# Kernel optimization log

Hardware: AMD Instinct MI355X
Metric: run time of the kernel (lower is better)

## Reference

```python
import jax, jax.numpy as jnp
import numpy as np

IH, IW = 32, 32
HEADS = 8
DIM_HEAD = 64
SCALE = DIM_HEAD ** -0.5


def _make_relative_index():
    # Matches torch buffer: ceil Euclidean distance between all pairs of 2D coords.
    ii, jj = np.meshgrid(np.arange(IH), np.arange(IW), indexing='ij')
    coords = np.stack([ii.ravel(), jj.ravel()])  # [2, n]
    rel = coords[:, :, None] - coords[:, None, :]  # [2, n, n]
    dist = np.ceil(np.sqrt(rel[0] ** 2 + rel[1] ** 2))
    return jnp.asarray(dist.astype(np.int32).ravel())  # [n*n]


def setup_inputs() -> dict:
    key = jax.random.key(0)
    k1, k2, k3, k4 = jax.random.split(key, 4)
    b, n, inp = 32, IH * IW, 512
    inner = HEADS * DIM_HEAD
    diag = int(np.ceil(np.sqrt((IH - 1) ** 2 + (IW - 1) ** 2)))
    return {
        'x': jax.random.normal(k1, (b, n, inp), jnp.float32),
        'w_qkv': jax.random.normal(k2, (inp, inner * 3), jnp.float32) * (inp ** -0.5),
        'bias_table': jax.random.normal(k3, (diag + 1, HEADS), jnp.float32) * 0.02,
        'w_out': jax.random.normal(k4, (inner, 512), jnp.float32) * (inner ** -0.5),
        'b_out': jnp.zeros((512,), jnp.float32),
        'relative_index': _make_relative_index(),
    }


def reference(x, w_qkv, bias_table, w_out, b_out, relative_index):
    b, n, _ = x.shape
    qkv = x @ w_qkv  # [b, n, 3*inner]
    q, k, v = jnp.split(qkv, 3, axis=-1)
    def to_heads(t):
        return t.reshape(b, n, HEADS, DIM_HEAD).transpose(0, 2, 1, 3)  # b h n d
    q, k, v = to_heads(q), to_heads(k), to_heads(v)
    dots = jnp.einsum('bhid,bhjd->bhij', q, k) * SCALE  # [b, h, n, n]
    # gather relative bias: [n*n, h] -> [1, h, n, n]
    rel_bias = bias_table[relative_index].reshape(n, n, HEADS).transpose(2, 0, 1)
    attn = jax.nn.softmax(dots + rel_bias[None], axis=-1)
    out = jnp.einsum('bhij,bhjd->bhid', attn, v)  # b h n d
    out = out.transpose(0, 2, 1, 3).reshape(b, n, HEADS * DIM_HEAD)
    return out @ w_out + b_out
```

## Files before the change

kernel.cpp:

```cpp
#include <hip/hip_runtime.h>
#include <hip/hip_bf16.h>
#include <cstdint>

typedef __bf16 bf16_t;
typedef bf16_t bf16x8 __attribute__((ext_vector_type(8)));
typedef float f32x4 __attribute__((ext_vector_type(4)));
typedef float f32x16 __attribute__((ext_vector_type(16)));
typedef unsigned u32x4 __attribute__((ext_vector_type(4)));

#define MFMA16(a, b, c) __builtin_amdgcn_mfma_f32_16x16x32_bf16(a, b, c, 0, 0, 0)
#define MFMA32(a, b, c) __builtin_amdgcn_mfma_f32_32x32x16_bf16(a, b, c, 0, 0, 0)

constexpr int LDK = 72;

#define QSCALE 0.1803368801f
#define LOG2E 1.44269504f

__global__ void zero_out(unsigned short* __restrict__ out, long n) {
    long i = (long)blockIdx.x * 256 + threadIdx.x;
    if (i < n) out[i] = 0;
}

__global__ void detect_dtype(const unsigned* __restrict__ x,
                             int* __restrict__ flag) {
    if (threadIdx.x == 0 && blockIdx.x == 0) {
        int cnt = 0;
        for (int i = 0; i < 1024; ++i) {
            unsigned e = (x[i] >> 7) & 0xFF;
            cnt += (e > 100 && e < 150) ? 1 : 0;
        }
        *flag = (cnt > 512) ? 1 : 0;
    }
}

__global__ void transpose_flex(const void* __restrict__ in,
                               bf16_t* __restrict__ out, int R, int C,
                               const int* __restrict__ flagp, int scale_rows) {
    const int fl = *flagp;
    __shared__ bf16_t tile[32][33];
    int c0 = blockIdx.x * 32, r0 = blockIdx.y * 32;
    int x = threadIdx.x, y = threadIdx.y;
#pragma unroll
    for (int i = 0; i < 4; ++i) {
        long idx = (long)(r0 + y + 8 * i) * C + c0 + x;
        float fv = fl ? (float)((const bf16_t*)in)[idx]
                      : ((const float*)in)[idx];
        if (c0 + x < scale_rows) fv *= QSCALE;
        tile[y + 8 * i][x] = (bf16_t)fv;
    }
    __syncthreads();
#pragma unroll
    for (int i = 0; i < 4; ++i)
        out[(long)(c0 + y + 8 * i) * R + r0 + x] = tile[x][y + 8 * i];
}

__global__ __launch_bounds__(256) void build_bias_perm(
    const int* __restrict__ rel_index, const void* __restrict__ bias_table,
    bf16_t* __restrict__ perm, const int* __restrict__ flagp) {
    const int fl = *flagp;
    const int jt = blockIdx.x;
    const int qb = blockIdx.y;
    const int t = threadIdx.x;
    const int lane = t & 63;
    const int h = (t >> 6) + 4 * blockIdx.z;
    const int i = qb * 32 + (lane & 31);
    const int hi = lane >> 5;
    bf16_t out[16];
#pragma unroll
    for (int r = 0; r < 16; ++r) {
        int j = jt * 32 + (r & 3) + 8 * (r >> 2) + 4 * hi;
        int ridx = rel_index[i * 1024 + j];
        ridx = ridx < 0 ? 0 : (ridx > 44 ? 44 : ridx);
        float bv = fl ? (float)((const bf16_t*)bias_table)[ridx * 8 + h]
                      : ((const float*)bias_table)[ridx * 8 + h];
        out[r] = (bf16_t)(bv * LOG2E);
    }
    long off = (((long)(h * 32 + qb) * 32 + jt) << 10) + lane * 16;
    *(uint4*)&perm[off] = *(uint4*)&out[0];
    *(uint4*)&perm[off + 8] = *(uint4*)&out[8];
}

template <bool AFLEX, bool BIAS, bool OUTFLEX>
__global__ __launch_bounds__(256) void gemm128(
    const void* __restrict__ A, const bf16_t* __restrict__ Bt, int K, int lda,
    long a_row0, void* __restrict__ C, int ldc, long c_row0,
    const void* __restrict__ bias, const int* __restrict__ flagp) {
    const int fl = *flagp;
    __shared__ bf16_t a_lds[128 * LDK];
    __shared__ bf16_t b_lds[128 * LDK];
    int t = threadIdx.x;
    int wave = t >> 6, lane = t & 63;
    int m16 = lane & 15, quad = lane >> 4;
    int wr = wave >> 1, wc = wave & 1;
    long m0 = (long)blockIdx.y * 128;
    int n0 = blockIdx.x * 128;

    f32x4 acc[4][4] = {};

    for (int ks = 0; ks < K; ks += 64) {
#pragma unroll
        for (int i = 0; i < 4; ++i) {
            int c = t + 256 * i;
            int row = c >> 3;
            int kc = (c & 7) << 3;
            bf16x8 av;
            if (AFLEX && !fl) {
                const float* Af = (const float*)A;
                long base = (a_row0 + m0 + row) * (long)lda + ks + kc;
                f32x4 lo = *(const f32x4*)&Af[base];
                f32x4 hi = *(const f32x4*)&Af[base + 4];
#pragma unroll
                for (int e = 0; e < 4; ++e) {
                    av[e] = (bf16_t)lo[e];
                    av[e + 4] = (bf16_t)hi[e];
                }
            } else {
                av = *(const bf16x8*)&(
                    (const bf16_t*)A)[(a_row0 + m0 + row) * (long)lda + ks + kc];
            }
            *(bf16x8*)&a_lds[row * LDK + kc] = av;
            *(bf16x8*)&b_lds[row * LDK + kc] =
                *(const bf16x8*)&Bt[(long)(n0 + row) * K + ks + kc];
        }
        __syncthreads();
#pragma unroll
        for (int kf = 0; kf < 2; ++kf) {
            bf16x8 af[4], bfr[4];
#pragma unroll
            for (int mb = 0; mb < 4; ++mb)
                af[mb] = *(const bf16x8*)&a_lds[(wr * 64 + mb * 16 + m16) * LDK +
                                                kf * 32 + quad * 8];
#pragma unroll
            for (int nb = 0; nb < 4; ++nb)
                bfr[nb] = *(const bf16x8*)&b_lds[(wc * 64 + nb * 16 + m16) * LDK +
                                                 kf * 32 + quad * 8];
#pragma unroll
            for (int mb = 0; mb < 4; ++mb)
#pragma unroll
                for (int nb = 0; nb < 4; ++nb)
                    acc[mb][nb] = MFMA16(af[mb], bfr[nb], acc[mb][nb]);
        }
        __syncthreads();
    }

#pragma unroll
    for (int mb = 0; mb < 4; ++mb) {
#pragma unroll
        for (int nb = 0; nb < 4; ++nb) {
            int col = n0 + wc * 64 + nb * 16 + m16;
#pragma unroll
            for (int r = 0; r < 4; ++r) {
                long row = m0 + wr * 64 + mb * 16 + quad * 4 + r;
                float v = acc[mb][nb][r];
                if (BIAS) {
                    float bb = fl ? (float)((const bf16_t*)bias)[col]
                                  : ((const float*)bias)[col];
                    v += bb;
                }
                long off = (c_row0 + row) * (long)ldc + col;
                if (OUTFLEX && !fl)
                    ((float*)C)[off] = v;
                else
                    ((bf16_t*)C)[off] = (bf16_t)v;
            }
        }
    }
}

__global__ __launch_bounds__(256) void flash_attn2(
    bf16_t* __restrict__ qkv, const bf16_t* __restrict__ bias_perm) {
    __shared__ bf16_t k_lds[2][64 * 64];
    __shared__ bf16_t v_lds[2][64 * 64];

    const int t = threadIdx.x;
    const int lane = t & 63, wave = t >> 6;
    const int l31 = lane & 31, hi = lane >> 5;
    const int h = blockIdx.y, b = blockIdx.z;
    bf16_t* base = qkv + (long)b * 1024 * 1536;
    bf16_t* qb = base + h * 64;
    const bf16_t* kb = base + 512 + h * 64;
    const bf16_t* vb = base + 1024 + h * 64;
    const int qblk = blockIdx.x * 4 + wave;
    const int q0w = qblk * 32;
    const bf16_t* bp = bias_perm + (((long)(h * 32 + qblk)) << 15) + lane * 16;

    bf16x8 qf[4];
#pragma unroll
    for (int s = 0; s < 4; ++s)
        qf[s] = *(const bf16x8*)&qb[(long)(q0w + l31) * 1536 + s * 16 + hi * 8];

    f32x16 oacc0 = {}, oacc1 = {};
    float mrun = -1e30f, lrun = 0.f;

    const int sr0 = t >> 3, sg0 = t & 7;
    const int sr1 = sr0 + 32;

    {
        bf16x8 k0 = *(const bf16x8*)&kb[(long)sr0 * 1536 + sg0 * 8];
        bf16x8 k1 = *(const bf16x8*)&kb[(long)sr1 * 1536 + sg0 * 8];
        bf16x8 v0 = *(const bf16x8*)&vb[(long)sr0 * 1536 + sg0 * 8];
        bf16x8 v1 = *(const bf16x8*)&vb[(long)sr1 * 1536 + sg0 * 8];
        *(bf16x8*)&k_lds[0][sr0 * 64 + ((sg0 ^ (sr0 & 7)) << 3)] = k0;
        *(bf16x8*)&k_lds[0][sr1 * 64 + ((sg0 ^ (sr1 & 7)) << 3)] = k1;
#pragma unroll
        for (int e = 0; e < 8; ++e) {
            int d0 = sg0 * 8 + e;
            v_lds[0][d0 * 64 + (((sr0 >> 3) ^ (d0 & 7)) << 3) + (sr0 & 7)] = v0[e];
            v_lds[0][d0 * 64 + (((sr1 >> 3) ^ (d0 & 7)) << 3) + (sr1 & 7)] = v1[e];
        }
    }
    __syncthreads();

    for (int tt = 0; tt < 16; ++tt) {
        const int cur = tt & 1;
        bf16x8 kn0 = {}, kn1 = {}, vn0 = {}, vn1 = {};
        if (tt < 15) {
            long j0n = (long)(tt + 1) * 64;
            kn0 = *(const bf16x8*)&kb[(j0n + sr0) * 1536 + sg0 * 8];
            kn1 = *(const bf16x8*)&kb[(j0n + sr1) * 1536 + sg0 * 8];
            vn0 = *(const bf16x8*)&vb[(j0n + sr0) * 1536 + sg0 * 8];
            vn1 = *(const bf16x8*)&vb[(j0n + sr1) * 1536 + sg0 * 8];
        }
        const bf16_t* bt = bp + ((long)tt << 11);
        uint4 bv[4];
        bv[0] = *(const uint4*)(bt);
        bv[1] = *(const uint4*)(bt + 8);
        bv[2] = *(const uint4*)(bt + 1024);
        bv[3] = *(const uint4*)(bt + 1024 + 8);

#pragma unroll
        for (int js = 0; js < 2; ++js) {
            f32x16 s = {};
            const int krow = js * 32 + l31;
#pragma unroll
            for (int st = 0; st < 4; ++st) {
                bf16x8 kf = *(const bf16x8*)&k_lds[cur][krow * 64 +
                             (((st * 2 + hi) ^ (krow & 7)) << 3)];
                s = MFMA32(kf, qf[st], s);
            }
            bf16_t bb[16];
            *(uint4*)&bb[0] = bv[2 * js];
            *(uint4*)&bb[8] = bv[2 * js + 1];
            float sv[16];
#pragma unroll
            for (int r = 0; r < 16; ++r) sv[r] = s[r] + (float)bb[r];
            float mx = sv[0];
#pragma unroll
            for (int r = 1; r < 16; ++r) mx = fmaxf(mx, sv[r]);
            {
                float o0 = mx, o1 = mx;
                asm("" : "+v"(o1));
                asm("v_permlane32_swap_b32 %0, %1" : "+v"(o0), "+v"(o1));
                mx = fmaxf(o0, o1);
            }
            if (!__all(mx <= mrun + 11.0f)) {
                float mnew = fmaxf(mrun, mx);
                float al = __builtin_amdgcn_exp2f(mrun - mnew);
                mrun = mnew;
                lrun *= al;
#pragma unroll
                for (int r = 0; r < 16; ++r) {
                    oacc0[r] *= al;
                    oacc1[r] *= al;
                }
            }
            float s0 = 0.f, s1 = 0.f, s2 = 0.f, s3 = 0.f;
#pragma unroll
            for (int r = 0; r < 16; ++r) {
                sv[r] = __builtin_amdgcn_exp2f(sv[r] - mrun);
                if ((r & 3) == 0) s0 += sv[r];
                else if ((r & 3) == 1) s1 += sv[r];
                else if ((r & 3) == 2) s2 += sv[r];
                else s3 += sv[r];
            }
            float rs = (s0 + s1) + (s2 + s3);
            {
                float o0 = rs, o1 = rs;
                asm("" : "+v"(o1));
                asm("v_permlane32_swap_b32 %0, %1" : "+v"(o0), "+v"(o1));
                rs = o0 + o1;
            }
            lrun += rs;
            unsigned dw[8];
#pragma unroll
            for (int g = 0; g < 4; ++g) {
                unsigned da, db;
                asm("v_cvt_pk_bf16_f32 %0, %1, %2"
                    : "=v"(da) : "v"(sv[4 * g]), "v"(sv[4 * g + 1]));
                asm("v_cvt_pk_bf16_f32 %0, %1, %2"
                    : "=v"(db) : "v"(sv[4 * g + 2]), "v"(sv[4 * g + 3]));
                dw[2 * g] = da;
                dw[2 * g + 1] = db;
            }
#pragma unroll
            for (int kk = 0; kk < 2; ++kk) {
                asm("v_permlane32_swap_b32 %0, %1"
                    : "+v"(dw[4 * kk + 0]), "+v"(dw[4 * kk + 2]));
                asm("v_permlane32_swap_b32 %0, %1"
                    : "+v"(dw[4 * kk + 1]), "+v"(dw[4 * kk + 3]));
            }
#pragma unroll
            for (int kk = 0; kk < 2; ++kk) {
                u32x4 uv;
                uv[0] = dw[4 * kk + 0];
                uv[1] = dw[4 * kk + 1];
                uv[2] = dw[4 * kk + 2];
                uv[3] = dw[4 * kk + 3];
                bf16x8 pa = __builtin_bit_cast(bf16x8, uv);
#pragma unroll
                for (int db2 = 0; db2 < 2; ++db2) {
                    const int vrow = db2 * 32 + l31;
                    bf16x8 vf = *(const bf16x8*)&v_lds[cur][vrow * 64 +
                                 (((js * 4 + kk * 2 + hi) ^ (vrow & 7)) << 3)];
                    if (db2 == 0)
                        oacc0 = MFMA32(pa, vf, oacc0);
                    else
                        oacc1 = MFMA32(pa, vf, oacc1);
                }
            }
        }
        if (tt < 15) {
            const int nb = cur ^ 1;
            *(bf16x8*)&k_lds[nb][sr0 * 64 + ((sg0 ^ (sr0 & 7)) << 3)] = kn0;
            *(bf16x8*)&k_lds[nb][sr1 * 64 + ((sg0 ^ (sr1 & 7)) << 3)] = kn1;
#pragma unroll
            for (int e = 0; e < 8; ++e) {
                int d0 = sg0 * 8 + e;
                v_lds[nb][d0 * 64 + (((sr0 >> 3) ^ (d0 & 7)) << 3) + (sr0 & 7)] =
                    vn0[e];
                v_lds[nb][d0 * 64 + (((sr1 >> 3) ^ (d0 & 7)) << 3) + (sr1 & 7)] =
                    vn1[e];
            }
        }
        __syncthreads();
    }

    float linv = 1.0f / lrun;
#pragma unroll
    for (int r = 0; r < 16; ++r) {
        int row = (r & 3) + 8 * (r >> 2) + 4 * hi;
        float lr = __int_as_float(
            __builtin_amdgcn_ds_bpermute(row << 2, __float_as_int(linv)));
        qb[(long)(q0w + row) * 1536 + l31] = (bf16_t)(oacc0[r] * lr);
        qb[(long)(q0w + row) * 1536 + 32 + l31] = (bf16_t)(oacc1[r] * lr);
    }
}

extern "C" void kernel_launch(void* const* d_in, const int* in_sizes, int n_in,
                              void* d_out, int out_size, void* d_ws,
                              size_t ws_size, hipStream_t stream) {
    const void* x = nullptr;
    const void* w_qkv = nullptr;
    const void* bias_table = nullptr;
    const void* w_out = nullptr;
    const void* b_out = nullptr;
    const void* rel_raw = nullptr;
    for (int i = 0; i < n_in; ++i) {
        switch (in_sizes[i]) {
            case 16777216: x = d_in[i]; break;
            case 786432:  w_qkv = d_in[i]; break;
            case 360:     bias_table = d_in[i]; break;
            case 262144:  w_out = d_in[i]; break;
            case 512:     b_out = d_in[i]; break;
            case 1048576: rel_raw = d_in[i]; break;
            default: break;
        }
    }
    if (!x || !w_qkv || !bias_table || !w_out || !b_out || !rel_raw) {
        x = d_in[0]; w_qkv = d_in[1]; bias_table = d_in[2];
        w_out = d_in[3]; b_out = d_in[4]; rel_raw = d_in[5];
    }
    const int* rel_index = (const int*)rel_raw;

    char* ws = (char*)d_ws;
    bf16_t* wqkvT = (bf16_t*)ws;
    bf16_t* woutT = (bf16_t*)(ws + 1572864);
    int* flag = (int*)(ws + 1572864 + 524288);
    bf16_t* rel_bias = (bf16_t*)(ws + 1572864 + 524288 + 256);
    const size_t fixed = 1572864 + 524288 + 256 + 16777216;
    bf16_t* qkv = (bf16_t*)(ws + fixed);
    const size_t per_batch = (size_t)1024 * 1536 * sizeof(bf16_t);

    if (ws_size < fixed + per_batch) {
        long n = (long)out_size;
        long nblk = (n + 255) / 256;
        if (nblk > 0)
            zero_out<<<(unsigned)nblk, 256, 0, stream>>>(
                (unsigned short*)d_out, n);
        return;
    }

    size_t avail = ws_size - fixed;
    int chunk = (int)(avail / per_batch);
    if (chunk > 32) chunk = 32;
    if (chunk < 1) chunk = 1;
    while (32 % chunk) --chunk;

    detect_dtype<<<1, 64, 0, stream>>>((const unsigned*)x, flag);
    transpose_flex<<<dim3(1536 / 32, 512 / 32), dim3(32, 8), 0, stream>>>(
        w_qkv, wqkvT, 512, 1536, flag, 512);
    transpose_flex<<<dim3(512 / 32, 512 / 32), dim3(32, 8), 0, stream>>>(
        w_out, woutT, 512, 512, flag, 0);
    build_bias_perm<<<dim3(32, 32, 2), 256, 0, stream>>>(
        rel_index, bias_table, rel_bias, flag);

    for (int b0 = 0; b0 < 32; b0 += chunk) {
        long row0 = (long)b0 * 1024;
        int mrows = chunk * 1024;
        gemm128<true, false, false>
            <<<dim3(1536 / 128, mrows / 128), 256, 0, stream>>>(
                x, wqkvT, 512, 512, row0, qkv, 1536, 0, nullptr, flag);
        flash_attn2<<<dim3(8, 8, chunk), 256, 0, stream>>>(qkv, rel_bias);
        gemm128<false, true, true>
            <<<dim3(512 / 128, mrows / 128), 256, 0, stream>>>(
                qkv, woutT, 512, 1536, 0, d_out, 512, row0, b_out, flag);
    }
}
```

Before: 503.2 us.

## Pre-convert x to bf16 and use direct global-to-LDS loads in GEMMs

Measured after the change: 474.2 us. 5.8% less time.

```diff
diff --git a/kernel.cpp b/kernel.cpp
--- a/kernel.cpp
+++ b/kernel.cpp
@@ -10,6 +10,11 @@
 
 #define MFMA16(a, b, c) __builtin_amdgcn_mfma_f32_16x16x32_bf16(a, b, c, 0, 0, 0)
 #define MFMA32(a, b, c) __builtin_amdgcn_mfma_f32_32x32x16_bf16(a, b, c, 0, 0, 0)
+
+#define GLOAD_LDS16(g, l)                                                  \
+    __builtin_amdgcn_global_load_lds(                                      \
+        (const __attribute__((address_space(1))) unsigned*)(g),            \
+        (__attribute__((address_space(3))) unsigned*)(l), 16, 0, 0)
 
 constexpr int LDK = 72;
 
@@ -30,6 +35,26 @@
             cnt += (e > 100 && e < 150) ? 1 : 0;
         }
         *flag = (cnt > 512) ? 1 : 0;
+    }
+}
+
+__global__ __launch_bounds__(256) void convert_x(const void* __restrict__ in,
+                                                 bf16_t* __restrict__ out,
+                                                 const int* __restrict__ flagp) {
+    const int fl = *flagp;
+    long i = ((long)blockIdx.x * 256 + threadIdx.x) * 8;
+    if (fl) {
+        *(bf16x8*)&out[i] = *(const bf16x8*)&((const bf16_t*)in)[i];
+    } else {
+        f32x4 lo = *(const f32x4*)&((const float*)in)[i];
+        f32x4 hi = *(const f32x4*)&((const float*)in)[i + 4];
+        bf16x8 v;
+#pragma unroll
+        for (int e = 0; e < 4; ++e) {
+            v[e] = (bf16_t)lo[e];
+            v[e + 4] = (bf16_t)hi[e];
+        }
+        *(bf16x8*)&out[i] = v;
     }
 }
 
@@ -78,6 +103,81 @@
     long off = (((long)(h * 32 + qb) * 32 + jt) << 10) + lane * 16;
     *(uint4*)&perm[off] = *(uint4*)&out[0];
     *(uint4*)&perm[off + 8] = *(uint4*)&out[8];
+}
+
+template <bool BIAS, bool OUTFLEX>
+__global__ __launch_bounds__(256) void gemm_lds(
+    const bf16_t* __restrict__ A, const bf16_t* __restrict__ Bt, int K,
+    int lda, long a_row0, void* __restrict__ C, int ldc, long c_row0,
+    const void* __restrict__ bias, const int* __restrict__ flagp) {
+    const int fl = *flagp;
+    __shared__ bf16_t a_lds[128 * 64];
+    __shared__ bf16_t b_lds[128 * 64];
+    int t = threadIdx.x;
+    int wave = t >> 6, lane = t & 63;
+    int m16 = lane & 15, quad = lane >> 4;
+    int wr = wave >> 1, wc = wave & 1;
+    long m0 = (long)blockIdx.y * 128;
+    int n0 = blockIdx.x * 128;
+
+    const int c_base = wave * 256 + lane;
+
+    f32x4 acc[4][4] = {};
+
+    for (int ks = 0; ks < K; ks += 64) {
+#pragma unroll
+        for (int i = 0; i < 4; ++i) {
+            int c = c_base;
+            c = wave * 256 + i * 64 + lane;
+            int row = c >> 3, kc = (c & 7) << 3;
+            GLOAD_LDS16(&A[(a_row0 + m0 + row) * (long)lda + ks + kc],
+                        &a_lds[row * 64 + kc]);
+            GLOAD_LDS16(&Bt[(long)(n0 + row) * K + ks + kc],
+                        &b_lds[row * 64 + kc]);
+        }
+        __syncthreads();
+#pragma unroll
+        for (int kf = 0; kf < 2; ++kf) {
+            bf16x8 af[4], bfr[4];
+#pragma unroll
+            for (int mb = 0; mb < 4; ++mb)
+                af[mb] = *(const bf16x8*)&a_lds[(wr * 64 + mb * 16 + m16) * 64 +
+                                                kf * 32 + quad * 8];
+#pragma unroll
+            for (int nb = 0; nb < 4; ++nb)
+                bfr[nb] = *(const bf16x8*)&b_lds[(wc * 64 + nb * 16 + m16) * 64 +
+                                                 kf * 32 + quad * 8];
+#pragma unroll
+            for (int mb = 0; mb < 4; ++mb)
+#pragma unroll
+                for (int nb = 0; nb < 4; ++nb)
+                    acc[mb][nb] = MFMA16(af[mb], bfr[nb], acc[mb][nb]);
+        }
+        __syncthreads();
+    }
+
+#pragma unroll
+    for (int mb = 0; mb < 4; ++mb) {
+#pragma unroll
+        for (int nb = 0; nb < 4; ++nb) {
+            int col = n0 + wc * 64 + nb * 16 + m16;
+#pragma unroll
+            for (int r = 0; r < 4; ++r) {
+                long row = m0 + wr * 64 + mb * 16 + quad * 4 + r;
+                float v = acc[mb][nb][r];
+                if (BIAS) {
+                    float bb = fl ? (float)((const bf16_t*)bias)[col]
+                                  : ((const float*)bias)[col];
+                    v += bb;
+                }
+                long off = (c_row0 + row) * (long)ldc + col;
+                if (OUTFLEX && !fl)
+                    ((float*)C)[off] = v;
+                else
+                    ((bf16_t*)C)[off] = (bf16_t)v;
+            }
+        }
+    }
 }
 
 template <bool AFLEX, bool BIAS, bool OUTFLEX>
@@ -378,7 +478,7 @@
     int* flag = (int*)(ws + 1572864 + 524288);
     bf16_t* rel_bias = (bf16_t*)(ws + 1572864 + 524288 + 256);
     const size_t fixed = 1572864 + 524288 + 256 + 16777216;
-    bf16_t* qkv = (bf16_t*)(ws + fixed);
+    const size_t xbf_bytes = (size_t)32 * 1024 * 512 * sizeof(bf16_t);
     const size_t per_batch = (size_t)1024 * 1536 * sizeof(bf16_t);
 
     if (ws_size < fixed + per_batch) {
@@ -390,7 +490,12 @@
         return;
     }
 
-    size_t avail = ws_size - fixed;
+    bool have_xbf = ws_size >= fixed + xbf_bytes + per_batch;
+    bf16_t* x_bf = (bf16_t*)(ws + fixed);
+    bf16_t* qkv = have_xbf ? (bf16_t*)(ws + fixed + xbf_bytes)
+                           : (bf16_t*)(ws + fixed);
+
+    size_t avail = ws_size - fixed - (have_xbf ? xbf_bytes : 0);
     int chunk = (int)(avail / per_batch);
     if (chunk > 32) chunk = 32;
     if (chunk < 1) chunk = 1;
@@ -403,15 +508,23 @@
         w_out, woutT, 512, 512, flag, 0);
     build_bias_perm<<<dim3(32, 32, 2), 256, 0, stream>>>(
         rel_index, bias_table, rel_bias, flag);
+    if (have_xbf)
+        convert_x<<<8192, 256, 0, stream>>>(x, x_bf, flag);
 
     for (int b0 = 0; b0 < 32; b0 += chunk) {
         long row0 = (long)b0 * 1024;
         int mrows = chunk * 1024;
-        gemm128<true, false, false>
-            <<<dim3(1536 / 128, mrows / 128), 256, 0, stream>>>(
-                x, wqkvT, 512, 512, row0, qkv, 1536, 0, nullptr, flag);
+        if (have_xbf) {
+            gemm_lds<false, false>
+                <<<dim3(1536 / 128, mrows / 128), 256, 0, stream>>>(
+                    x_bf, wqkvT, 512, 512, row0, qkv, 1536, 0, nullptr, flag);
+        } else {
+            gemm128<true, false, false>
+                <<<dim3(1536 / 128, mrows / 128), 256, 0, stream>>>(
+                    x, wqkvT, 512, 512, row0, qkv, 1536, 0, nullptr, flag);
+        }
         flash_attn2<<<dim3(8, 8, chunk), 256, 0, stream>>>(qkv, rel_bias);
-        gemm128<false, true, true>
+        gemm_lds<true, true>
             <<<dim3(512 / 128, mrows / 128), 256, 0, stream>>>(
                 qkv, woutT, 512, 1536, 0, d_out, 512, row0, b_out, flag);
     }
```
